# Performance work log

Measured on AMD Instinct MI355X. Metric: run time of the kernel, lower is better.

## Reference

```python
import jax, jax.numpy as jnp
import numpy as np

POOL = 2
H, W, C = 128, 128, 64  # expected_shape


def _bpca_pool_single(x):
    """x: [H, W, C] -> [H//POOL, W//POOL, C], replicating TF BPCAPooling math."""
    h2, w2 = H // POOL, W // POOL
    # tf.image.extract_patches flattens each 2x2 patch in (dy, dx, ch) order;
    # the subsequent reshape to [H*W*(C//4), 4] therefore groups 4 consecutive
    # channels at a fixed spatial offset per row. Replicate exactly:
    p = x.reshape(h2, POOL, w2, POOL, C).transpose(0, 2, 1, 3, 4)  # [h2,w2,2,2,C]
    patches = p.reshape(-1, POOL * POOL)  # [H*W*C/4, 4]
    # per-column standardization (population std, matching tf.math.reduce_std)
    mean = jnp.mean(patches, axis=0)
    std = jnp.std(patches, axis=0)
    denom = jnp.where(std == 0, 1.0, std)
    patches = jnp.where(std == 0, 0.0, (patches - mean) / denom)  # NaN->0 as in TF
    # top-1 right singular vector of patches == top eigenvector of 4x4 Gram;
    # avoids a full tall-skinny SVD (same math as tf.linalg.svd route).
    gram = patches.T @ patches  # [4, 4]
    _, vecs = jnp.linalg.eigh(gram)  # ascending eigenvalues
    v = vecs[:, -1:]  # [4, 1] top principal direction (n_components=1)
    v = v * jnp.where(jnp.sum(v) < 0, -1.0, 1.0)  # fix SVD sign ambiguity
    out = patches @ v  # [H*W*C/4, 1]
    return out.reshape(h2, w2, C)


def setup_inputs() -> dict:
    key = jax.random.key(0)
    inputs = jax.random.normal(key, (32, H, W, C), dtype=jnp.float32)
    return {"inputs": inputs}


def reference(inputs):
    return jax.vmap(_bpca_pool_single)(inputs)  # [B, H//2, W//2, C]
```

## Files before the change

kernel.cpp:

```cpp
#include <hip/hip_runtime.h>
#include <math.h>


#define NBATCH 32
#define N_PER_BATCH (128 * 128 * 64)
#define ROWS_PER_BATCH (N_PER_BATCH / 4)
#define BLOCKS_PER_BATCH 64
#define ROWS_PER_BLOCK (ROWS_PER_BATCH / BLOCKS_PER_BATCH)
#define ROWS_PER_THREAD (ROWS_PER_BLOCK / 256)

#define WB_OFFSET (2048 * 14 * 8)

__device__ inline double wave_reduce_add(double v) {
    #pragma unroll
    for (int off = 32; off > 0; off >>= 1) v += __shfl_down(v, off, 64);
    return v;
}

__global__ __launch_bounds__(256) void stats_kernel(const float* __restrict__ in,
                                                    double* __restrict__ partials) {
    const int batch = blockIdx.x / BLOCKS_PER_BATCH;
    const int chunk = blockIdx.x % BLOCKS_PER_BATCH;
    const float4* src = (const float4*)(in + (size_t)batch * N_PER_BATCH);
    const int base = chunk * ROWS_PER_BLOCK + threadIdx.x;

    double s0 = 0, s1 = 0, s2 = 0, s3 = 0;
    double p00 = 0, p01 = 0, p02 = 0, p03 = 0;
    double p11 = 0, p12 = 0, p13 = 0;
    double p22 = 0, p23 = 0, p33 = 0;

    #pragma unroll 4
    for (int k = 0; k < ROWS_PER_THREAD; ++k) {
        float4 v = src[base + k * 256];
        double a = (double)v.x, b = (double)v.y, c = (double)v.z, d = (double)v.w;
        s0 += a; s1 += b; s2 += c; s3 += d;
        p00 += a * a; p01 += a * b; p02 += a * c; p03 += a * d;
        p11 += b * b; p12 += b * c; p13 += b * d;
        p22 += c * c; p23 += c * d; p33 += d * d;
    }

    double vals[14] = {s0, s1, s2, s3, p00, p01, p02, p03, p11, p12, p13, p22, p23, p33};
    __shared__ double red[4][14];
    const int lane = threadIdx.x & 63;
    const int wave = threadIdx.x >> 6;
    #pragma unroll
    for (int i = 0; i < 14; ++i) {
        double r = wave_reduce_add(vals[i]);
        if (lane == 0) red[wave][i] = r;
    }
    __syncthreads();
    if (threadIdx.x < 14) {
        partials[(size_t)blockIdx.x * 14 + threadIdx.x] =
            red[0][threadIdx.x] + red[1][threadIdx.x] +
            red[2][threadIdx.x] + red[3][threadIdx.x];
    }
}

__global__ __launch_bounds__(64) void eigen_kernel(const double* __restrict__ partials,
                                                   float* __restrict__ wb) {
    const int b = blockIdx.x;
    const double* p = partials + ((size_t)b * 64 + threadIdx.x) * 14;

    double a[14];
    #pragma unroll
    for (int i = 0; i < 14; ++i) a[i] = wave_reduce_add(p[i]);

    if (threadIdx.x != 0) return;

    const double N = (double)ROWS_PER_BATCH;
    double sum[4] = {a[0], a[1], a[2], a[3]};
    double S[4][4];
    S[0][0] = a[4];  S[0][1] = S[1][0] = a[5];  S[0][2] = S[2][0] = a[6];  S[0][3] = S[3][0] = a[7];
    S[1][1] = a[8];  S[1][2] = S[2][1] = a[9];  S[1][3] = S[3][1] = a[10];
    S[2][2] = a[11]; S[2][3] = S[3][2] = a[12]; S[3][3] = a[13];

    double m[4], sd[4], dn[4];
    #pragma unroll
    for (int j = 0; j < 4; ++j) {
        m[j] = sum[j] / N;
        double var = S[j][j] / N - m[j] * m[j];
        if (var < 0.0) var = 0.0;
        sd[j] = sqrt(var);
        dn[j] = (sd[j] == 0.0) ? 1.0 : sd[j];
    }

    double A[4][4];
    #pragma unroll
    for (int j = 0; j < 4; ++j)
        #pragma unroll
        for (int k = 0; k < 4; ++k) {
            if (sd[j] == 0.0 || sd[k] == 0.0) A[j][k] = 0.0;
            else A[j][k] = (S[j][k] / N - m[j] * m[k]) / (dn[j] * dn[k]);
        }

    double V[4][4] = {{1, 0, 0, 0}, {0, 1, 0, 0}, {0, 0, 1, 0}, {0, 0, 0, 1}};
    for (int sweep = 0; sweep < 6; ++sweep) {
        for (int pp = 0; pp < 3; ++pp) {
            for (int q = pp + 1; q < 4; ++q) {
                double apq = A[pp][q];
                if (fabs(apq) < 1e-300) continue;
                double theta = (A[q][q] - A[pp][pp]) / (2.0 * apq);
                double t = copysign(1.0, theta) / (fabs(theta) + sqrt(theta * theta + 1.0));
                double c = 1.0 / sqrt(t * t + 1.0);
                double s = t * c;
                for (int k = 0; k < 4; ++k) {
                    double t1 = A[k][pp], t2 = A[k][q];
                    A[k][pp] = c * t1 - s * t2;
                    A[k][q]  = s * t1 + c * t2;
                }
                for (int k = 0; k < 4; ++k) {
                    double t1 = A[pp][k], t2 = A[q][k];
                    A[pp][k] = c * t1 - s * t2;
                    A[q][k]  = s * t1 + c * t2;
                }
                for (int k = 0; k < 4; ++k) {
                    double t1 = V[k][pp], t2 = V[k][q];
                    V[k][pp] = c * t1 - s * t2;
                    V[k][q]  = s * t1 + c * t2;
                }
            }
        }
    }

    int jmax = 0;
    double emax = A[0][0];
    for (int j = 1; j < 4; ++j)
        if (A[j][j] > emax) { emax = A[j][j]; jmax = j; }
    double v[4] = {V[0][jmax], V[1][jmax], V[2][jmax], V[3][jmax]};
    double sv = v[0] + v[1] + v[2] + v[3];
    if (sv < 0.0) { v[0] = -v[0]; v[1] = -v[1]; v[2] = -v[2]; v[3] = -v[3]; }

    double w[4], bias = 0.0;
    #pragma unroll
    for (int j = 0; j < 4; ++j) {
        w[j] = (sd[j] == 0.0) ? 0.0 : v[j] / dn[j];
        bias -= w[j] * m[j];
    }
    float* o = wb + b * 8;
    o[0] = (float)w[0]; o[1] = (float)w[1]; o[2] = (float)w[2]; o[3] = (float)w[3];
    o[4] = (float)bias;
}

__global__ __launch_bounds__(256) void proj_kernel(const float* __restrict__ in,
                                                   const float* __restrict__ wb,
                                                   float4* __restrict__ out) {
    const int t = blockIdx.x * 256 + threadIdx.x;
    const int b  = t >> 16;
    const int r4 = t & 65535;
    const int i0 = r4 >> 10;
    const int i1 = (r4 >> 4) & 63;
    const int c0 = (r4 & 15) * 4;
    const int i2 = c0 >> 5;
    const int i3 = (c0 >> 4) & 1;
    const int g0 = c0 & 15;

    const float* src = in + (size_t)(((b * 128 + 2 * i0 + i2) * 128) + (2 * i1 + i3)) * 64
                          + 4 * g0;
    const float4* s4 = (const float4*)src;
    float4 x0 = s4[0], x1 = s4[1], x2 = s4[2], x3 = s4[3];

    const float* p = wb + b * 8;
    float w0 = p[0], w1 = p[1], w2 = p[2], w3 = p[3], bias = p[4];

    float4 o;
    o.x = fmaf(w0, x0.x, fmaf(w1, x0.y, fmaf(w2, x0.z, fmaf(w3, x0.w, bias))));
    o.y = fmaf(w0, x1.x, fmaf(w1, x1.y, fmaf(w2, x1.z, fmaf(w3, x1.w, bias))));
    o.z = fmaf(w0, x2.x, fmaf(w1, x2.y, fmaf(w2, x2.z, fmaf(w3, x2.w, bias))));
    o.w = fmaf(w0, x3.x, fmaf(w1, x3.y, fmaf(w2, x3.z, fmaf(w3, x3.w, bias))));
    out[t] = o;
}

extern "C" void kernel_launch(void* const* d_in, const int* in_sizes, int n_in,
                              void* d_out, int out_size, void* d_ws, size_t ws_size,
                              hipStream_t stream) {
    const float* in = (const float*)d_in[0];
    float* out = (float*)d_out;
    double* partials = (double*)d_ws;
    float* wb = (float*)((char*)d_ws + WB_OFFSET);

    stats_kernel<<<NBATCH * BLOCKS_PER_BATCH, 256, 0, stream>>>(in, partials);
    eigen_kernel<<<NBATCH, 64, 0, stream>>>(partials, wb);
    proj_kernel<<<(NBATCH * ROWS_PER_BATCH / 4) / 256, 256, 0, stream>>>(in, wb, (float4*)out);
}
```

Before: 252.1 us.

## Fuse eigen solve into stats kernel via last-block atomic counter

Removes the separate eigen_kernel launch: each stats block bumps a per-batch atomic counter, and the last block to finish a batch reduces that batch's partials and runs the 4x4 Jacobi eigen solve inline. A memset of the counters is added to the stream, and the Jacobi sweep count drops from 6 to 4, with launch_bounds occupancy hints added. The aim is to cut one kernel launch and its dependency gap, at the cost of a memset launch, fence/atomic overhead and slightly fewer Jacobi iterations.

Result: slower. 318.8 us (+26.5%).

```diff
diff --git a/kernel.cpp b/kernel.cpp
--- a/kernel.cpp
+++ b/kernel.cpp
@@ -9,7 +9,8 @@
 #define ROWS_PER_BLOCK (ROWS_PER_BATCH / BLOCKS_PER_BATCH)
 #define ROWS_PER_THREAD (ROWS_PER_BLOCK / 256)
 
-#define WB_OFFSET (2048 * 14 * 8)
+#define CNT_OFFSET (2048 * 14 * 8)
+#define WB_OFFSET (CNT_OFFSET + 128)
 
 __device__ inline double wave_reduce_add(double v) {
     #pragma unroll
@@ -17,8 +18,10 @@
     return v;
 }
 
-__global__ __launch_bounds__(256) void stats_kernel(const float* __restrict__ in,
-                                                    double* __restrict__ partials) {
+__global__ __launch_bounds__(256, 4) void stats_kernel(const float* __restrict__ in,
+                                                       double* __restrict__ partials,
+                                                       unsigned int* __restrict__ counters,
+                                                       float* __restrict__ wb) {
     const int batch = blockIdx.x / BLOCKS_PER_BATCH;
     const int chunk = blockIdx.x % BLOCKS_PER_BATCH;
     const float4* src = (const float4*)(in + (size_t)batch * N_PER_BATCH);
@@ -41,6 +44,7 @@
 
     double vals[14] = {s0, s1, s2, s3, p00, p01, p02, p03, p11, p12, p13, p22, p23, p33};
     __shared__ double red[4][14];
+    __shared__ int is_last;
     const int lane = threadIdx.x & 63;
     const int wave = threadIdx.x >> 6;
     #pragma unroll
@@ -53,19 +57,23 @@
         partials[(size_t)blockIdx.x * 14 + threadIdx.x] =
             red[0][threadIdx.x] + red[1][threadIdx.x] +
             red[2][threadIdx.x] + red[3][threadIdx.x];
+        __threadfence();
     }
-}
+    __syncthreads();
+    if (threadIdx.x == 0) {
+        unsigned int old = atomicAdd(&counters[batch], 1u);
+        is_last = (old == BLOCKS_PER_BATCH - 1);
+    }
+    __syncthreads();
+    if (!is_last || threadIdx.x >= 64) return;
 
-__global__ __launch_bounds__(64) void eigen_kernel(const double* __restrict__ partials,
-                                                   float* __restrict__ wb) {
-    const int b = blockIdx.x;
-    const double* p = partials + ((size_t)b * 64 + threadIdx.x) * 14;
-
+    __threadfence();
+    const double* p = partials + ((size_t)batch * BLOCKS_PER_BATCH + lane) * 14;
     double a[14];
     #pragma unroll
     for (int i = 0; i < 14; ++i) a[i] = wave_reduce_add(p[i]);
 
-    if (threadIdx.x != 0) return;
+    if (lane != 0) return;
 
     const double N = (double)ROWS_PER_BATCH;
     double sum[4] = {a[0], a[1], a[2], a[3]};
@@ -94,7 +102,7 @@
         }
 
     double V[4][4] = {{1, 0, 0, 0}, {0, 1, 0, 0}, {0, 0, 1, 0}, {0, 0, 0, 1}};
-    for (int sweep = 0; sweep < 6; ++sweep) {
+    for (int sweep = 0; sweep < 4; ++sweep) {
         for (int pp = 0; pp < 3; ++pp) {
             for (int q = pp + 1; q < 4; ++q) {
                 double apq = A[pp][q];
@@ -136,7 +144,7 @@
         w[j] = (sd[j] == 0.0) ? 0.0 : v[j] / dn[j];
         bias -= w[j] * m[j];
     }
-    float* o = wb + b * 8;
+    float* o = wb + batch * 8;
     o[0] = (float)w[0]; o[1] = (float)w[1]; o[2] = (float)w[2]; o[3] = (float)w[3];
     o[4] = (float)bias;
 }
@@ -174,11 +182,12 @@
                               void* d_out, int out_size, void* d_ws, size_t ws_size,
                               hipStream_t stream) {
     const float* in = (const float*)d_in[0];
-    float* out = (float*)d_out;
+    float4* out = (float4*)d_out;
     double* partials = (double*)d_ws;
+    unsigned int* counters = (unsigned int*)((char*)d_ws + CNT_OFFSET);
     float* wb = (float*)((char*)d_ws + WB_OFFSET);
 
-    stats_kernel<<<NBATCH * BLOCKS_PER_BATCH, 256, 0, stream>>>(in, partials);
-    eigen_kernel<<<NBATCH, 64, 0, stream>>>(partials, wb);
+    hipMemsetAsync(counters, 0, NBATCH * sizeof(unsigned int), stream);
+    stats_kernel<<<NBATCH * BLOCKS_PER_BATCH, 256, 0, stream>>>(in, partials, counters, wb);
     proj_kernel<<<(NBATCH * ROWS_PER_BATCH / 4) / 256, 256, 0, stream>>>(in, wb, (float4*)out);
 }
```
